# Kernel optimization log

Measured on AMD Instinct MI355X. Metric: run time of the kernel, lower is better.

## Reference

```python
import jax, jax.numpy as jnp
import numpy as np

DIM, H, KV, HD, WIN = 1024, 16, 4, 64, 512
EPS = 1e-6


def rmsnorm(x, w, eps=EPS):
    # torch.nn.RMSNorm: x * rsqrt(mean(x^2, -1) + eps) * w
    return x * jax.lax.rsqrt(jnp.mean(x * x, axis=-1, keepdims=True) + eps) * w


def setup_inputs() -> dict:
    key = jax.random.key(0)
    ks = jax.random.split(key, 7)
    B, T = 4, 2048
    s = 0.02
    return {
        "x": jax.random.normal(ks[0], (B, T, DIM), dtype=jnp.float32),
        "wq": jax.random.normal(ks[1], (H * HD, DIM), dtype=jnp.float32) * s,
        "wk": jax.random.normal(ks[2], (KV * HD, DIM), dtype=jnp.float32) * s,
        "wv": jax.random.normal(ks[3], (KV * HD, DIM), dtype=jnp.float32) * s,
        "wo": jax.random.normal(ks[4], (DIM, H * HD), dtype=jnp.float32) * s,
        "q_norm_w": jnp.ones((HD,), dtype=jnp.float32),
        "k_norm_w": jnp.ones((HD,), dtype=jnp.float32),
    }


def reference(x, wq, wk, wv, wo, q_norm_w, k_norm_w):
    B, T, D = x.shape
    rep = H // KV
    q = (x @ wq.T).reshape(B, T, H, HD)
    k = (x @ wk.T).reshape(B, T, KV, HD)
    v = (x @ wv.T).reshape(B, T, KV, HD)
    q = rmsnorm(q, q_norm_w)
    k = rmsnorm(k, k_norm_w)
    # GQA repeat: each kv head repeated `rep` times contiguously
    k = jnp.repeat(k, rep, axis=2)  # [B,T,H,HD]
    v = jnp.repeat(v, rep, axis=2)
    # scores [B,H,T,T]
    scores = jnp.einsum('bqhd,bkhd->bhqk', q, k) / jnp.sqrt(jnp.float32(HD))
    i = jnp.arange(T)[:, None]
    j = jnp.arange(T)[None, :]
    mask = (i >= j) & (i - j < WIN)  # causal sliding window band
    scores = jnp.where(mask, scores, -jnp.inf)
    attn = jax.nn.softmax(scores, axis=-1)
    y = jnp.einsum('bhqk,bkhd->bqhd', attn, v).reshape(B, T, H * HD)
    return y @ wo.T
```

## Files before the change

kernel.cpp:

```cpp
#include <hip/hip_runtime.h>
#include <hip/hip_bf16.h>

#define DIMD 1024
#define NH   16
#define NKV  4
#define HDIM 64
#define WINSZ 512
#define BB   4
#define TT   2048
#define MROWS (BB*TT)
#define NQKV 1536

typedef __attribute__((ext_vector_type(8))) short short8;
typedef __attribute__((ext_vector_type(4))) float f32x4;

static __device__ __forceinline__ short f2bf(float f) {
  __hip_bfloat16 h = __float2bfloat16(f);
  return __builtin_bit_cast(short, h);
}
static __device__ __forceinline__ float bf2f(short s) {
  return __bfloat162float(__builtin_bit_cast(__hip_bfloat16, s));
}
static __device__ __forceinline__ unsigned pk2(float a, float b) {
  unsigned lo = (unsigned short)f2bf(a);
  unsigned hi = (unsigned short)f2bf(b);
  return lo | (hi << 16);
}

static __device__ __forceinline__ void gld_lds16(const void* g, void* l) {
  __builtin_amdgcn_global_load_lds(
      (const __attribute__((address_space(1))) unsigned int*)g,
      (__attribute__((address_space(3))) unsigned int*)l, 16, 0, 0);
}

template<int N>
static __device__ __forceinline__ float dpp_ror(float x) {
  return __builtin_bit_cast(float, __builtin_amdgcn_update_dpp(
      0, __builtin_bit_cast(int, x), 0x120 + N, 0xF, 0xF, true));
}

__global__ __launch_bounds__(256) void cvt_all_kernel(
    const float* __restrict__ x, const float* __restrict__ wq,
    const float* __restrict__ wk, const float* __restrict__ wv,
    const float* __restrict__ wo,
    short* __restrict__ xb, short* __restrict__ wqkvb, short* __restrict__ wob) {
  size_t u = (size_t)blockIdx.x * 256 + threadIdx.x;
  const float* src; short* dst;
  if (u < 2097152)                   { src = x;  dst = xb; }
  else if ((u -= 2097152) < 262144)  { src = wq; dst = wqkvb; }
  else if ((u -= 262144) < 65536)    { src = wk; dst = wqkvb + 1024*1024; }
  else if ((u -= 65536) < 65536)     { src = wv; dst = wqkvb + 1280*1024; }
  else { u -= 65536;                   src = wo; dst = wob; }
  float4 v = ((const float4*)src)[u];
  short4 o;
  o.x = f2bf(v.x); o.y = f2bf(v.y); o.z = f2bf(v.z); o.w = f2bf(v.w);
  ((short4*)dst)[u] = o;
}

#define BMT 128
#define BNT 128
#define BKT 64

template<bool OUT_BF16>
__global__ __launch_bounds__(256) void gemm_bt(
    const short* __restrict__ A, const short* __restrict__ Bw,
    void* __restrict__ Cout, int M, int N, int K) {
  __shared__ __align__(16) short As[BMT*BKT];
  __shared__ __align__(16) short Bs[BNT*BKT];

  int nwg  = gridDim.x;
  int orig = blockIdx.x;
  int wg   = (orig & 7) * (nwg >> 3) + (orig >> 3);
  int tiles_n = N / BNT;
  int m0 = (wg / tiles_n) * BMT;
  int n0 = (wg % tiles_n) * BNT;

  int tid = threadIdx.x;
  int lane = tid & 63, wv = tid >> 6;
  int l15 = lane & 15, lg = lane >> 4;
  int wr = wv >> 1, wc = wv & 1;

  f32x4 acc[4][4] = {};

  for (int k0 = 0; k0 < K; k0 += BKT) {
    __syncthreads();
    const char* Abase = (const char*)(A + (size_t)m0 * K + k0);
    const char* Bbase = (const char*)(Bw + (size_t)n0 * K + k0);
#pragma unroll
    for (int i = 0; i < 4; ++i) {
      int idx = i * 256 + tid;
      int row = idx >> 3;
      int cb  = (idx & 7) << 4;
      int scb = cb ^ ((row & 7) << 4);
      gld_lds16(Abase + (size_t)row * (K * 2) + scb,
                (char*)As + ((i * 256 + wv * 64) << 4));
      gld_lds16(Bbase + (size_t)row * (K * 2) + scb,
                (char*)Bs + ((i * 256 + wv * 64) << 4));
    }
    __syncthreads();

#pragma unroll
    for (int kk = 0; kk < 2; ++kk) {
      short8 af[4], bfr[4];
      int kb = (kk * 32 + lg * 8) * 2;
#pragma unroll
      for (int mi = 0; mi < 4; ++mi) {
        int row = wr * 64 + mi * 16 + l15;
        af[mi] = *(const short8*)((const char*)As + row * 128 + (kb ^ ((row & 7) << 4)));
      }
#pragma unroll
      for (int ni = 0; ni < 4; ++ni) {
        int row = wc * 64 + ni * 16 + l15;
        bfr[ni] = *(const short8*)((const char*)Bs + row * 128 + (kb ^ ((row & 7) << 4)));
      }
#pragma unroll
      for (int mi = 0; mi < 4; ++mi)
#pragma unroll
        for (int ni = 0; ni < 4; ++ni)
          acc[mi][ni] = __builtin_amdgcn_mfma_f32_16x16x32_bf16(af[mi], bfr[ni], acc[mi][ni], 0, 0, 0);
    }
  }

  int crow0 = m0 + wr * 64, ccol0 = n0 + wc * 64;
#pragma unroll
  for (int mi = 0; mi < 4; ++mi)
#pragma unroll
    for (int ni = 0; ni < 4; ++ni)
#pragma unroll
      for (int r = 0; r < 4; ++r) {
        int row = crow0 + mi * 16 + lg * 4 + r;
        int col = ccol0 + ni * 16 + l15;
        float v = acc[mi][ni][r];
        if (OUT_BF16) ((short*)Cout)[(size_t)row * N + col] = f2bf(v);
        else          ((float*)Cout)[(size_t)row * N + col] = v;
      }
}

__global__ __launch_bounds__(256) void qk_norm_kernel(
    const short* __restrict__ qkv, const float* __restrict__ qw,
    const float* __restrict__ kw, short* __restrict__ Qh, short* __restrict__ Kh) {
  unsigned gid = blockIdx.x * 16u + (threadIdx.x >> 4);
  int l = threadIdx.x & 15;
  unsigned row = gid / 20u;
  int s = (int)(gid - row * 20u);
  int b = row >> 11, t = row & 2047;
  bool isq = s < 16;
  int col = isq ? s * 64 : 1024 + (s - 16) * 64;
  const short* rp = qkv + (size_t)row * NQKV + col + l * 4;
  short4 v4 = *(const short4*)rp;
  float f0 = bf2f(v4.x), f1 = bf2f(v4.y), f2 = bf2f(v4.z), f3 = bf2f(v4.w);
  float ss = f0 * f0 + f1 * f1 + f2 * f2 + f3 * f3;
  ss += dpp_ror<1>(ss); ss += dpp_ror<2>(ss);
  ss += dpp_ror<4>(ss); ss += dpp_ror<8>(ss);
  float r = rsqrtf(ss * (1.0f / 64.0f) + 1e-6f);
  float4 w4 = *(const float4*)((isq ? qw : kw) + l * 4);
  short4 o;
  o.x = f2bf(f0 * r * w4.x); o.y = f2bf(f1 * r * w4.y);
  o.z = f2bf(f2 * r * w4.z); o.w = f2bf(f3 * r * w4.w);
  if (isq) *(short4*)(Qh + (((size_t)b * NH + s) * TT + t) * HDIM + l * 4) = o;
  else     *(short4*)(Kh + (((size_t)b * NKV + (s - 16)) * TT + t) * HDIM + l * 4) = o;
}

__global__ __launch_bounds__(256) void vtrans_kernel(
    const short* __restrict__ qkv, short* __restrict__ Vt) {
  int tb = blockIdx.x, kv = blockIdx.y, b = blockIdx.z;
  __shared__ short tile[64][72];
  int tid = threadIdx.x;
#pragma unroll
  for (int i = 0; i < 2; ++i) {
    int idx = i * 256 + tid;
    int tr = idx >> 3;
    int c8 = (idx & 7) * 8;
    int t = tb * 64 + tr;
    const short* src = qkv + (size_t)(b * TT + t) * NQKV + 1280 + kv * 64 + c8;
    short8 v = *(const short8*)src;
#pragma unroll
    for (int j = 0; j < 8; ++j) tile[tr][c8 + j] = v[j];
  }
  __syncthreads();
#pragma unroll
  for (int i = 0; i < 2; ++i) {
    int idx = i * 256 + tid;
    int d = idx >> 3;
    int t8 = (idx & 7) * 8;
    short8 o;
#pragma unroll
    for (int j = 0; j < 8; ++j) o[j] = tile[t8 + j][d];
    short* dst = Vt + (((size_t)(b * NKV + kv) * HDIM) + d) * TT + tb * 64 + t8;
    *(short8*)dst = o;
  }
}

#define C1A 0.180336880f
#define C2A 11.5415603f

__global__ __launch_bounds__(256) void attn_kernel(
    const short* __restrict__ Qh, const short* __restrict__ Kh,
    const short* __restrict__ Vt, short* __restrict__ Y) {
  int wgid = blockIdx.x;
  int qh = wgid >> 4;
  int kvh = (wgid >> 2) & 3;
  int b = wgid & 3;
  int tid = threadIdx.x, lane = tid & 63, wv = tid >> 6;
  int l15 = lane & 15, lg = lane >> 4;
  int h = kvh * 4 + wv;
  int q0 = qh * 32;
  const short* Qp = Qh + (((size_t)b * NH + h) * TT + q0) * HDIM;
  const char*  Kp = (const char*)(Kh + ((size_t)b * NKV + kvh) * TT * HDIM);
  const char*  Vp = (const char*)(Vt + ((size_t)b * NKV + kvh) * HDIM * TT);

  short8 aqA0 = *(const short8*)(Qp + l15 * HDIM + lg * 8);
  short8 aqA1 = *(const short8*)(Qp + l15 * HDIM + 32 + lg * 8);
  short8 aqB0 = *(const short8*)(Qp + (16 + l15) * HDIM + lg * 8);
  short8 aqB1 = *(const short8*)(Qp + (16 + l15) * HDIM + 32 + lg * 8);

  float lpA = 0.f, lpB = 0.f;
  f32x4 yA[4] = {}, yB[4] = {};

  __shared__ __align__(16) char smem[34816];
  char* Kbuf = smem;
  char* Vbuf = smem + 8192;
  short* PA = (short*)(smem + 16384 + wv * 4608);
  short* PB = PA + 1152;

  int lo = q0 - (WINSZ - 1); if (lo < 0) lo = 0;
  int klo = lo & ~63;
  int nt = (q0 + 32 - klo + 63) >> 6;

  int qiA = q0 + l15, qiB = qiA + 16;

  for (int t = 0; t < nt; ++t) {
    int kc = klo + t * 64;
    __syncthreads();
#pragma unroll
    for (int r = 0; r < 2; ++r) {
      int rr = wv * 16 + r * 8 + (lane >> 3);
      int cb = (lane & 7) * 16;
      int scb = cb ^ ((rr & 7) << 4);
      gld_lds16(Kp + (size_t)(kc + rr) * 128 + scb,
                Kbuf + wv * 2048 + r * 1024);
      gld_lds16(Vp + (size_t)rr * (TT * 2) + kc * 2 + scb,
                Vbuf + wv * 2048 + r * 1024);
    }
    __syncthreads();

    int sw = (l15 & 7) << 4;
    short8 bk0[4], bk1[4];
#pragma unroll
    for (int nc = 0; nc < 4; ++nc) {
      int rb = (nc * 16 + l15) * 128;
      bk0[nc] = *(const short8*)(Kbuf + rb + ((lg * 16) ^ sw));
      bk1[nc] = *(const short8*)(Kbuf + rb + ((lg * 16 + 64) ^ sw));
    }
    short8 bv0[4], bv1[4];
#pragma unroll
    for (int dt = 0; dt < 4; ++dt) {
      int rb = (dt * 16 + l15) * 128;
      bv0[dt] = *(const short8*)(Vbuf + rb + ((lg * 16) ^ sw));
      bv1[dt] = *(const short8*)(Vbuf + rb + ((lg * 16 + 64) ^ sw));
    }
    f32x4 sA[4], sB[4];
    __builtin_amdgcn_s_setprio(1);
#pragma unroll
    for (int nc = 0; nc < 4; ++nc) {
      f32x4 zA = {}, zB = {};
      zA = __builtin_amdgcn_mfma_f32_16x16x32_bf16(bk0[nc], aqA0, zA, 0, 0, 0);
      zB = __builtin_amdgcn_mfma_f32_16x16x32_bf16(bk0[nc], aqB0, zB, 0, 0, 0);
      zA = __builtin_amdgcn_mfma_f32_16x16x32_bf16(bk1[nc], aqA1, zA, 0, 0, 0);
      zB = __builtin_amdgcn_mfma_f32_16x16x32_bf16(bk1[nc], aqB1, zB, 0, 0, 0);
      sA[nc] = zA; sB[nc] = zB;
    }
    __builtin_amdgcn_s_setprio(0);
    bool intA = (kc >= q0 - 496) && (kc + 63 <= q0);
    bool intB = (kc >= q0 - 480) && (kc + 63 <= q0 + 16);
    if (intA && intB) {
#pragma unroll
      for (int nc = 0; nc < 4; ++nc) {
        float pa0 = __builtin_amdgcn_exp2f(fmaf(sA[nc][0], C1A, -C2A));
        float pa1 = __builtin_amdgcn_exp2f(fmaf(sA[nc][1], C1A, -C2A));
        float pa2 = __builtin_amdgcn_exp2f(fmaf(sA[nc][2], C1A, -C2A));
        float pa3 = __builtin_amdgcn_exp2f(fmaf(sA[nc][3], C1A, -C2A));
        float pb0 = __builtin_amdgcn_exp2f(fmaf(sB[nc][0], C1A, -C2A));
        float pb1 = __builtin_amdgcn_exp2f(fmaf(sB[nc][1], C1A, -C2A));
        float pb2 = __builtin_amdgcn_exp2f(fmaf(sB[nc][2], C1A, -C2A));
        float pb3 = __builtin_amdgcn_exp2f(fmaf(sB[nc][3], C1A, -C2A));
        lpA += (pa0 + pa1) + (pa2 + pa3);
        lpB += (pb0 + pb1) + (pb2 + pb3);
        *(uint2*)(PA + l15 * 72 + nc * 16 + lg * 4) = uint2{pk2(pa0, pa1), pk2(pa2, pa3)};
        *(uint2*)(PB + l15 * 72 + nc * 16 + lg * 4) = uint2{pk2(pb0, pb1), pk2(pb2, pb3)};
      }
    } else {
      int kjb = kc + lg * 4;
#pragma unroll
      for (int nc = 0; nc < 4; ++nc) {
        float pa[4], pb[4];
#pragma unroll
        for (int r = 0; r < 4; ++r) {
          int kj = kjb + nc * 16 + r;
          bool okA = (kj <= qiA) && (qiA - kj < WINSZ);
          bool okB = (kj <= qiB) && (qiB - kj < WINSZ);
          pa[r] = okA ? __builtin_amdgcn_exp2f(fmaf(sA[nc][r], C1A, -C2A)) : 0.f;
          pb[r] = okB ? __builtin_amdgcn_exp2f(fmaf(sB[nc][r], C1A, -C2A)) : 0.f;
        }
        lpA += (pa[0] + pa[1]) + (pa[2] + pa[3]);
        lpB += (pb[0] + pb[1]) + (pb[2] + pb[3]);
        *(uint2*)(PA + l15 * 72 + nc * 16 + lg * 4) = uint2{pk2(pa[0], pa[1]), pk2(pa[2], pa[3])};
        *(uint2*)(PB + l15 * 72 + nc * 16 + lg * 4) = uint2{pk2(pb[0], pb[1]), pk2(pb[2], pb[3])};
      }
    }
    short8 apA0 = *(const short8*)(PA + l15 * 72 + lg * 8);
    short8 apA1 = *(const short8*)(PA + l15 * 72 + 32 + lg * 8);
    short8 apB0 = *(const short8*)(PB + l15 * 72 + lg * 8);
    short8 apB1 = *(const short8*)(PB + l15 * 72 + 32 + lg * 8);
    __builtin_amdgcn_s_setprio(1);
#pragma unroll
    for (int dt = 0; dt < 4; ++dt) {
      yA[dt] = __builtin_amdgcn_mfma_f32_16x16x32_bf16(apA0, bv0[dt], yA[dt], 0, 0, 0);
      yB[dt] = __builtin_amdgcn_mfma_f32_16x16x32_bf16(apB0, bv0[dt], yB[dt], 0, 0, 0);
      yA[dt] = __builtin_amdgcn_mfma_f32_16x16x32_bf16(apA1, bv1[dt], yA[dt], 0, 0, 0);
      yB[dt] = __builtin_amdgcn_mfma_f32_16x16x32_bf16(apB1, bv1[dt], yB[dt], 0, 0, 0);
    }
    __builtin_amdgcn_s_setprio(0);
  }

  lpA += __shfl_xor(lpA, 16); lpA += __shfl_xor(lpA, 32);
  lpB += __shfl_xor(lpB, 16); lpB += __shfl_xor(lpB, 32);
  float invqA = 1.0f / lpA;
  float invqB = 1.0f / lpB;
#pragma unroll
  for (int r = 0; r < 4; ++r) {
    float invA = __builtin_bit_cast(float, __builtin_amdgcn_ds_bpermute(
        (lg * 4 + r) << 2, __builtin_bit_cast(int, invqA)));
    float invB = __builtin_bit_cast(float, __builtin_amdgcn_ds_bpermute(
        (lg * 4 + r) << 2, __builtin_bit_cast(int, invqB)));
    int qiAo = q0 + lg * 4 + r, qiBo = qiAo + 16;
#pragma unroll
    for (int dt = 0; dt < 4; ++dt) {
      Y[((size_t)(b * TT + qiAo)) * DIMD + h * HDIM + dt * 16 + l15] = f2bf(yA[dt][r] * invA);
      Y[((size_t)(b * TT + qiBo)) * DIMD + h * HDIM + dt * 16 + l15] = f2bf(yB[dt][r] * invB);
    }
  }
}

extern "C" void kernel_launch(void* const* d_in, const int* in_sizes, int n_in,
                              void* d_out, int out_size, void* d_ws, size_t ws_size,
                              hipStream_t stream) {
  const float* x  = (const float*)d_in[0];
  const float* wq = (const float*)d_in[1];
  const float* wk = (const float*)d_in[2];
  const float* wv = (const float*)d_in[3];
  const float* wo = (const float*)d_in[4];
  const float* qw = (const float*)d_in[5];
  const float* kw = (const float*)d_in[6];

  char* ws = (char*)d_ws;
  short* xb    = (short*)(ws + 0);
  short* wqkvb = (short*)(ws + 16777216);
  short* wob   = (short*)(ws + 19922944);
  short* qkv   = (short*)(ws + 22020096);
  short* Qh    = (short*)(ws + 47185920);
  short* Kh    = (short*)(ws + 63963136);
  short* Vt    = (short*)(ws + 68157440);
  short* Y     = xb;
  float* outp  = (float*)d_out;

  cvt_all_kernel<<<10752, 256, 0, stream>>>(x, wq, wk, wv, wo, xb, wqkvb, wob);
  gemm_bt<true><<<dim3(64 * 12), 256, 0, stream>>>(xb, wqkvb, (void*)qkv, MROWS, NQKV, DIMD);
  qk_norm_kernel<<<10240, 256, 0, stream>>>(qkv, qw, kw, Qh, Kh);
  vtrans_kernel<<<dim3(32, 4, 4), 256, 0, stream>>>(qkv, Vt);
  attn_kernel<<<1024, 256, 0, stream>>>(Qh, Kh, Vt, Y);
  gemm_bt<false><<<dim3(64 * 8), 256, 0, stream>>>(Y, wob, (void*)outp, MROWS, DIMD, DIMD);
}
```

Measured before the change: 120.0 us.

## Merge qk-norm and V-transpose launches; load 128-key tiles per barrier in attention

Combines the QK RMSNorm kernel and the V transpose kernel into one launch, with block index ranges selecting the role, which removes one kernel launch and its gap. The attention kernel now stages 128 keys of K and V per pair of barriers instead of 64 and processes them as two 64-key sub-steps, halving the number of block-wide syncs and load phases. When the last chunk holds only 64 keys, the extra loads are redirected to duplicate valid rows. Shared memory grows from about 34KB to 50KB, which may reduce how many blocks fit on each CU.

```diff
diff --git a/kernel.cpp b/kernel.cpp
--- a/kernel.cpp
+++ b/kernel.cpp
@@ -136,58 +136,59 @@
       }
 }
 
-__global__ __launch_bounds__(256) void qk_norm_kernel(
+__global__ __launch_bounds__(256) void norm_vtrans_kernel(
     const short* __restrict__ qkv, const float* __restrict__ qw,
-    const float* __restrict__ kw, short* __restrict__ Qh, short* __restrict__ Kh) {
-  unsigned gid = blockIdx.x * 16u + (threadIdx.x >> 4);
-  int l = threadIdx.x & 15;
-  unsigned row = gid / 20u;
-  int s = (int)(gid - row * 20u);
-  int b = row >> 11, t = row & 2047;
-  bool isq = s < 16;
-  int col = isq ? s * 64 : 1024 + (s - 16) * 64;
-  const short* rp = qkv + (size_t)row * NQKV + col + l * 4;
-  short4 v4 = *(const short4*)rp;
-  float f0 = bf2f(v4.x), f1 = bf2f(v4.y), f2 = bf2f(v4.z), f3 = bf2f(v4.w);
-  float ss = f0 * f0 + f1 * f1 + f2 * f2 + f3 * f3;
-  ss += dpp_ror<1>(ss); ss += dpp_ror<2>(ss);
-  ss += dpp_ror<4>(ss); ss += dpp_ror<8>(ss);
-  float r = rsqrtf(ss * (1.0f / 64.0f) + 1e-6f);
-  float4 w4 = *(const float4*)((isq ? qw : kw) + l * 4);
-  short4 o;
-  o.x = f2bf(f0 * r * w4.x); o.y = f2bf(f1 * r * w4.y);
-  o.z = f2bf(f2 * r * w4.z); o.w = f2bf(f3 * r * w4.w);
-  if (isq) *(short4*)(Qh + (((size_t)b * NH + s) * TT + t) * HDIM + l * 4) = o;
-  else     *(short4*)(Kh + (((size_t)b * NKV + (s - 16)) * TT + t) * HDIM + l * 4) = o;
-}
-
-__global__ __launch_bounds__(256) void vtrans_kernel(
-    const short* __restrict__ qkv, short* __restrict__ Vt) {
-  int tb = blockIdx.x, kv = blockIdx.y, b = blockIdx.z;
+    const float* __restrict__ kw, short* __restrict__ Qh,
+    short* __restrict__ Kh, short* __restrict__ Vt) {
   __shared__ short tile[64][72];
-  int tid = threadIdx.x;
-#pragma unroll
-  for (int i = 0; i < 2; ++i) {
-    int idx = i * 256 + tid;
-    int tr = idx >> 3;
-    int c8 = (idx & 7) * 8;
-    int t = tb * 64 + tr;
-    const short* src = qkv + (size_t)(b * TT + t) * NQKV + 1280 + kv * 64 + c8;
-    short8 v = *(const short8*)src;
-#pragma unroll
-    for (int j = 0; j < 8; ++j) tile[tr][c8 + j] = v[j];
-  }
-  __syncthreads();
-#pragma unroll
-  for (int i = 0; i < 2; ++i) {
-    int idx = i * 256 + tid;
-    int d = idx >> 3;
-    int t8 = (idx & 7) * 8;
-    short8 o;
-#pragma unroll
-    for (int j = 0; j < 8; ++j) o[j] = tile[t8 + j][d];
-    short* dst = Vt + (((size_t)(b * NKV + kv) * HDIM) + d) * TT + tb * 64 + t8;
-    *(short8*)dst = o;
+  if (blockIdx.x < 10240) {
+    unsigned gid = blockIdx.x * 16u + (threadIdx.x >> 4);
+    int l = threadIdx.x & 15;
+    unsigned row = gid / 20u;
+    int s = (int)(gid - row * 20u);
+    int b = row >> 11, t = row & 2047;
+    bool isq = s < 16;
+    int col = isq ? s * 64 : 1024 + (s - 16) * 64;
+    const short* rp = qkv + (size_t)row * NQKV + col + l * 4;
+    short4 v4 = *(const short4*)rp;
+    float f0 = bf2f(v4.x), f1 = bf2f(v4.y), f2 = bf2f(v4.z), f3 = bf2f(v4.w);
+    float ss = f0 * f0 + f1 * f1 + f2 * f2 + f3 * f3;
+    ss += dpp_ror<1>(ss); ss += dpp_ror<2>(ss);
+    ss += dpp_ror<4>(ss); ss += dpp_ror<8>(ss);
+    float r = rsqrtf(ss * (1.0f / 64.0f) + 1e-6f);
+    float4 w4 = *(const float4*)((isq ? qw : kw) + l * 4);
+    short4 o;
+    o.x = f2bf(f0 * r * w4.x); o.y = f2bf(f1 * r * w4.y);
+    o.z = f2bf(f2 * r * w4.z); o.w = f2bf(f3 * r * w4.w);
+    if (isq) *(short4*)(Qh + (((size_t)b * NH + s) * TT + t) * HDIM + l * 4) = o;
+    else     *(short4*)(Kh + (((size_t)b * NKV + (s - 16)) * TT + t) * HDIM + l * 4) = o;
+  } else {
+    int vi = blockIdx.x - 10240;
+    int tb = vi & 31, kv = (vi >> 5) & 3, b = vi >> 7;
+    int tid = threadIdx.x;
+#pragma unroll
+    for (int i = 0; i < 2; ++i) {
+      int idx = i * 256 + tid;
+      int tr = idx >> 3;
+      int c8 = (idx & 7) * 8;
+      int t = tb * 64 + tr;
+      const short* src = qkv + (size_t)(b * TT + t) * NQKV + 1280 + kv * 64 + c8;
+      short8 v = *(const short8*)src;
+#pragma unroll
+      for (int j = 0; j < 8; ++j) tile[tr][c8 + j] = v[j];
+    }
+    __syncthreads();
+#pragma unroll
+    for (int i = 0; i < 2; ++i) {
+      int idx = i * 256 + tid;
+      int d = idx >> 3;
+      int t8 = (idx & 7) * 8;
+      short8 o;
+#pragma unroll
+      for (int j = 0; j < 8; ++j) o[j] = tile[t8 + j][d];
+      short* dst = Vt + (((size_t)(b * NKV + kv) * HDIM) + d) * TT + tb * 64 + t8;
+      *(short8*)dst = o;
+    }
   }
 }
 
@@ -217,110 +218,119 @@
   float lpA = 0.f, lpB = 0.f;
   f32x4 yA[4] = {}, yB[4] = {};
 
-  __shared__ __align__(16) char smem[34816];
+  __shared__ __align__(16) char smem[51200];
   char* Kbuf = smem;
-  char* Vbuf = smem + 8192;
-  short* PA = (short*)(smem + 16384 + wv * 4608);
+  char* Vbuf = smem + 16384;
+  short* PA = (short*)(smem + 32768 + wv * 4608);
   short* PB = PA + 1152;
 
   int lo = q0 - (WINSZ - 1); if (lo < 0) lo = 0;
   int klo = lo & ~63;
-  int nt = (q0 + 32 - klo + 63) >> 6;
+  int khi = q0 + 32;
 
   int qiA = q0 + l15, qiB = qiA + 16;
 
-  for (int t = 0; t < nt; ++t) {
-    int kc = klo + t * 64;
-    __syncthreads();
-#pragma unroll
-    for (int r = 0; r < 2; ++r) {
-      int rr = wv * 16 + r * 8 + (lane >> 3);
-      int cb = (lane & 7) * 16;
-      int scb = cb ^ ((rr & 7) << 4);
-      gld_lds16(Kp + (size_t)(kc + rr) * 128 + scb,
-                Kbuf + wv * 2048 + r * 1024);
-      gld_lds16(Vp + (size_t)rr * (TT * 2) + kc * 2 + scb,
-                Vbuf + wv * 2048 + r * 1024);
+  for (int kc0 = klo; kc0 < khi; kc0 += 128) {
+    bool two = (kc0 + 64 < khi);
+    __syncthreads();
+#pragma unroll
+    for (int r = 0; r < 4; ++r) {
+      int rrk = wv * 32 + r * 8 + (lane >> 3);
+      int cbk = (lane & 7) * 16;
+      int rowk = (!two && rrk >= 64) ? (rrk - 64) : rrk;
+      gld_lds16(Kp + (size_t)(kc0 + rowk) * 128 + (cbk ^ ((rowk & 7) << 4)),
+                Kbuf + wv * 4096 + r * 1024);
+      int rrv = wv * 16 + r * 4 + (lane >> 4);
+      int cbv = (lane & 15) * 16;
+      int scbv = cbv ^ ((rrv & 7) << 4);
+      int adj = (!two && (cbv & 128)) ? 128 : 0;
+      gld_lds16(Vp + (size_t)rrv * (TT * 2) + kc0 * 2 + scbv - adj,
+                Vbuf + wv * 4096 + r * 1024);
     }
     __syncthreads();
 
     int sw = (l15 & 7) << 4;
-    short8 bk0[4], bk1[4];
-#pragma unroll
-    for (int nc = 0; nc < 4; ++nc) {
-      int rb = (nc * 16 + l15) * 128;
-      bk0[nc] = *(const short8*)(Kbuf + rb + ((lg * 16) ^ sw));
-      bk1[nc] = *(const short8*)(Kbuf + rb + ((lg * 16 + 64) ^ sw));
-    }
-    short8 bv0[4], bv1[4];
-#pragma unroll
-    for (int dt = 0; dt < 4; ++dt) {
-      int rb = (dt * 16 + l15) * 128;
-      bv0[dt] = *(const short8*)(Vbuf + rb + ((lg * 16) ^ sw));
-      bv1[dt] = *(const short8*)(Vbuf + rb + ((lg * 16 + 64) ^ sw));
-    }
-    f32x4 sA[4], sB[4];
-    __builtin_amdgcn_s_setprio(1);
-#pragma unroll
-    for (int nc = 0; nc < 4; ++nc) {
-      f32x4 zA = {}, zB = {};
-      zA = __builtin_amdgcn_mfma_f32_16x16x32_bf16(bk0[nc], aqA0, zA, 0, 0, 0);
-      zB = __builtin_amdgcn_mfma_f32_16x16x32_bf16(bk0[nc], aqB0, zB, 0, 0, 0);
-      zA = __builtin_amdgcn_mfma_f32_16x16x32_bf16(bk1[nc], aqA1, zA, 0, 0, 0);
-      zB = __builtin_amdgcn_mfma_f32_16x16x32_bf16(bk1[nc], aqB1, zB, 0, 0, 0);
-      sA[nc] = zA; sB[nc] = zB;
-    }
-    __builtin_amdgcn_s_setprio(0);
-    bool intA = (kc >= q0 - 496) && (kc + 63 <= q0);
-    bool intB = (kc >= q0 - 480) && (kc + 63 <= q0 + 16);
-    if (intA && intB) {
+#pragma unroll
+    for (int ts = 0; ts < 2; ++ts) {
+      if (ts && !two) break;
+      int kc = kc0 + ts * 64;
+      short8 bk0[4], bk1[4];
 #pragma unroll
       for (int nc = 0; nc < 4; ++nc) {
-        float pa0 = __builtin_amdgcn_exp2f(fmaf(sA[nc][0], C1A, -C2A));
-        float pa1 = __builtin_amdgcn_exp2f(fmaf(sA[nc][1], C1A, -C2A));
-        float pa2 = __builtin_amdgcn_exp2f(fmaf(sA[nc][2], C1A, -C2A));
-        float pa3 = __builtin_amdgcn_exp2f(fmaf(sA[nc][3], C1A, -C2A));
-        float pb0 = __builtin_amdgcn_exp2f(fmaf(sB[nc][0], C1A, -C2A));
-        float pb1 = __builtin_amdgcn_exp2f(fmaf(sB[nc][1], C1A, -C2A));
-        float pb2 = __builtin_amdgcn_exp2f(fmaf(sB[nc][2], C1A, -C2A));
-        float pb3 = __builtin_amdgcn_exp2f(fmaf(sB[nc][3], C1A, -C2A));
-        lpA += (pa0 + pa1) + (pa2 + pa3);
-        lpB += (pb0 + pb1) + (pb2 + pb3);
-        *(uint2*)(PA + l15 * 72 + nc * 16 + lg * 4) = uint2{pk2(pa0, pa1), pk2(pa2, pa3)};
-        *(uint2*)(PB + l15 * 72 + nc * 16 + lg * 4) = uint2{pk2(pb0, pb1), pk2(pb2, pb3)};
-      }
-    } else {
-      int kjb = kc + lg * 4;
+        int rb = (ts * 64 + nc * 16 + l15) * 128;
+        bk0[nc] = *(const short8*)(Kbuf + rb + ((lg * 16) ^ sw));
+        bk1[nc] = *(const short8*)(Kbuf + rb + ((lg * 16 + 64) ^ sw));
+      }
+      short8 bv0[4], bv1[4];
+#pragma unroll
+      for (int dt = 0; dt < 4; ++dt) {
+        int rb = (dt * 16 + l15) * 256 + ts * 128;
+        bv0[dt] = *(const short8*)(Vbuf + rb + ((lg * 16) ^ sw));
+        bv1[dt] = *(const short8*)(Vbuf + rb + ((lg * 16 + 64) ^ sw));
+      }
+      f32x4 sA[4], sB[4];
+      __builtin_amdgcn_s_setprio(1);
 #pragma unroll
       for (int nc = 0; nc < 4; ++nc) {
-        float pa[4], pb[4];
-#pragma unroll
-        for (int r = 0; r < 4; ++r) {
-          int kj = kjb + nc * 16 + r;
-          bool okA = (kj <= qiA) && (qiA - kj < WINSZ);
-          bool okB = (kj <= qiB) && (qiB - kj < WINSZ);
-          pa[r] = okA ? __builtin_amdgcn_exp2f(fmaf(sA[nc][r], C1A, -C2A)) : 0.f;
-          pb[r] = okB ? __builtin_amdgcn_exp2f(fmaf(sB[nc][r], C1A, -C2A)) : 0.f;
+        f32x4 zA = {}, zB = {};
+        zA = __builtin_amdgcn_mfma_f32_16x16x32_bf16(bk0[nc], aqA0, zA, 0, 0, 0);
+        zB = __builtin_amdgcn_mfma_f32_16x16x32_bf16(bk0[nc], aqB0, zB, 0, 0, 0);
+        zA = __builtin_amdgcn_mfma_f32_16x16x32_bf16(bk1[nc], aqA1, zA, 0, 0, 0);
+        zB = __builtin_amdgcn_mfma_f32_16x16x32_bf16(bk1[nc], aqB1, zB, 0, 0, 0);
+        sA[nc] = zA; sB[nc] = zB;
+      }
+      __builtin_amdgcn_s_setprio(0);
+      bool intA = (kc >= q0 - 496) && (kc + 63 <= q0);
+      bool intB = (kc >= q0 - 480) && (kc + 63 <= q0 + 16);
+      if (intA && intB) {
+#pragma unroll
+        for (int nc = 0; nc < 4; ++nc) {
+          float pa0 = __builtin_amdgcn_exp2f(fmaf(sA[nc][0], C1A, -C2A));
+          float pa1 = __builtin_amdgcn_exp2f(fmaf(sA[nc][1], C1A, -C2A));
+          float pa2 = __builtin_amdgcn_exp2f(fmaf(sA[nc][2], C1A, -C2A));
+          float pa3 = __builtin_amdgcn_exp2f(fmaf(sA[nc][3], C1A, -C2A));
+          float pb0 = __builtin_amdgcn_exp2f(fmaf(sB[nc][0], C1A, -C2A));
+          float pb1 = __builtin_amdgcn_exp2f(fmaf(sB[nc][1], C1A, -C2A));
+          float pb2 = __builtin_amdgcn_exp2f(fmaf(sB[nc][2], C1A, -C2A));
+          float pb3 = __builtin_amdgcn_exp2f(fmaf(sB[nc][3], C1A, -C2A));
+          lpA += (pa0 + pa1) + (pa2 + pa3);
+          lpB += (pb0 + pb1) + (pb2 + pb3);
+          *(uint2*)(PA + l15 * 72 + nc * 16 + lg * 4) = uint2{pk2(pa0, pa1), pk2(pa2, pa3)};
+          *(uint2*)(PB + l15 * 72 + nc * 16 + lg * 4) = uint2{pk2(pb0, pb1), pk2(pb2, pb3)};
         }
-        lpA += (pa[0] + pa[1]) + (pa[2] + pa[3]);
-        lpB += (pb[0] + pb[1]) + (pb[2] + pb[3]);
-        *(uint2*)(PA + l15 * 72 + nc * 16 + lg * 4) = uint2{pk2(pa[0], pa[1]), pk2(pa[2], pa[3])};
-        *(uint2*)(PB + l15 * 72 + nc * 16 + lg * 4) = uint2{pk2(pb[0], pb[1]), pk2(pb[2], pb[3])};
-      }
-    }
-    short8 apA0 = *(const short8*)(PA + l15 * 72 + lg * 8);
-    short8 apA1 = *(const short8*)(PA + l15 * 72 + 32 + lg * 8);
-    short8 apB0 = *(const short8*)(PB + l15 * 72 + lg * 8);
-    short8 apB1 = *(const short8*)(PB + l15 * 72 + 32 + lg * 8);
-    __builtin_amdgcn_s_setprio(1);
-#pragma unroll
-    for (int dt = 0; dt < 4; ++dt) {
-      yA[dt] = __builtin_amdgcn_mfma_f32_16x16x32_bf16(apA0, bv0[dt], yA[dt], 0, 0, 0);
-      yB[dt] = __builtin_amdgcn_mfma_f32_16x16x32_bf16(apB0, bv0[dt], yB[dt], 0, 0, 0);
-      yA[dt] = __builtin_amdgcn_mfma_f32_16x16x32_bf16(apA1, bv1[dt], yA[dt], 0, 0, 0);
-      yB[dt] = __builtin_amdgcn_mfma_f32_16x16x32_bf16(apB1, bv1[dt], yB[dt], 0, 0, 0);
-    }
-    __builtin_amdgcn_s_setprio(0);
+      } else {
+        int kjb = kc + lg * 4;
+#pragma unroll
+        for (int nc = 0; nc < 4; ++nc) {
+          float pa[4], pb[4];
+#pragma unroll
+          for (int r = 0; r < 4; ++r) {
+            int kj = kjb + nc * 16 + r;
+            bool okA = (kj <= qiA) && (qiA - kj < WINSZ);
+            bool okB = (kj <= qiB) && (qiB - kj < WINSZ);
+            pa[r] = okA ? __builtin_amdgcn_exp2f(fmaf(sA[nc][r], C1A, -C2A)) : 0.f;
+            pb[r] = okB ? __builtin_amdgcn_exp2f(fmaf(sB[nc][r], C1A, -C2A)) : 0.f;
+          }
+          lpA += (pa[0] + pa[1]) + (pa[2] + pa[3]);
+          lpB += (pb[0] + pb[1]) + (pb[2] + pb[3]);
+          *(uint2*)(PA + l15 * 72 + nc * 16 + lg * 4) = uint2{pk2(pa[0], pa[1]), pk2(pa[2], pa[3])};
+          *(uint2*)(PB + l15 * 72 + nc * 16 + lg * 4) = uint2{pk2(pb[0], pb[1]), pk2(pb[2], pb[3])};
+        }
+      }
+      short8 apA0 = *(const short8*)(PA + l15 * 72 + lg * 8);
+      short8 apA1 = *(const short8*)(PA + l15 * 72 + 32 + lg * 8);
+      short8 apB0 = *(const short8*)(PB + l15 * 72 + lg * 8);
+      short8 apB1 = *(const short8*)(PB + l15 * 72 + 32 + lg * 8);
+      __builtin_amdgcn_s_setprio(1);
+#pragma unroll
+      for (int dt = 0; dt < 4; ++dt) {
+        yA[dt] = __builtin_amdgcn_mfma_f32_16x16x32_bf16(apA0, bv0[dt], yA[dt], 0, 0, 0);
+        yB[dt] = __builtin_amdgcn_mfma_f32_16x16x32_bf16(apB0, bv0[dt], yB[dt], 0, 0, 0);
+        yA[dt] = __builtin_amdgcn_mfma_f32_16x16x32_bf16(apA1, bv1[dt], yA[dt], 0, 0, 0);
+        yB[dt] = __builtin_amdgcn_mfma_f32_16x16x32_bf16(apB1, bv1[dt], yB[dt], 0, 0, 0);
+      }
+      __builtin_amdgcn_s_setprio(0);
+    }
   }
 
   lpA += __shfl_xor(lpA, 16); lpA += __shfl_xor(lpA, 32);
@@ -366,8 +376,7 @@
 
   cvt_all_kernel<<<10752, 256, 0, stream>>>(x, wq, wk, wv, wo, xb, wqkvb, wob);
   gemm_bt<true><<<dim3(64 * 12), 256, 0, stream>>>(xb, wqkvb, (void*)qkv, MROWS, NQKV, DIMD);
-  qk_norm_kernel<<<10240, 256, 0, stream>>>(qkv, qw, kw, Qh, Kh);
-  vtrans_kernel<<<dim3(32, 4, 4), 256, 0, stream>>>(qkv, Vt);
+  norm_vtrans_kernel<<<10752, 256, 0, stream>>>(qkv, qw, kw, Qh, Kh, Vt);
   attn_kernel<<<1024, 256, 0, stream>>>(Qh, Kh, Vt, Y);
   gemm_bt<false><<<dim3(64 * 8), 256, 0, stream>>>(Y, wob, (void*)outp, MROWS, DIMD, DIMD);
 }
```

Measured after the change: 119.7 us. No clear change (-0.3%).

## Merge QK-norm and V-transpose kernels; split softmax/PV per query half

Applied to the files above, without the earlier changes.

The separate qk_norm and vtrans launches become one kernel, using block index ranges to pick the role, which removes one launch and its drain gap. In the attention inner loop, the A and B query sub-tiles are now handled one after the other, each with its own interior/boundary check and its own PV MFMA pass. The aim is to take the fast unmasked path more often and to interleave exp work with MFMA issue. The merged kernel reserves LDS for every block, including the norm blocks that never use it, and the extra branching adds some control overhead.

```diff
diff --git a/kernel.cpp b/kernel.cpp
--- a/kernel.cpp
+++ b/kernel.cpp
@@ -136,58 +136,59 @@
       }
 }
 
-__global__ __launch_bounds__(256) void qk_norm_kernel(
+__global__ __launch_bounds__(256) void norm_vtrans_kernel(
     const short* __restrict__ qkv, const float* __restrict__ qw,
-    const float* __restrict__ kw, short* __restrict__ Qh, short* __restrict__ Kh) {
-  unsigned gid = blockIdx.x * 16u + (threadIdx.x >> 4);
-  int l = threadIdx.x & 15;
-  unsigned row = gid / 20u;
-  int s = (int)(gid - row * 20u);
-  int b = row >> 11, t = row & 2047;
-  bool isq = s < 16;
-  int col = isq ? s * 64 : 1024 + (s - 16) * 64;
-  const short* rp = qkv + (size_t)row * NQKV + col + l * 4;
-  short4 v4 = *(const short4*)rp;
-  float f0 = bf2f(v4.x), f1 = bf2f(v4.y), f2 = bf2f(v4.z), f3 = bf2f(v4.w);
-  float ss = f0 * f0 + f1 * f1 + f2 * f2 + f3 * f3;
-  ss += dpp_ror<1>(ss); ss += dpp_ror<2>(ss);
-  ss += dpp_ror<4>(ss); ss += dpp_ror<8>(ss);
-  float r = rsqrtf(ss * (1.0f / 64.0f) + 1e-6f);
-  float4 w4 = *(const float4*)((isq ? qw : kw) + l * 4);
-  short4 o;
-  o.x = f2bf(f0 * r * w4.x); o.y = f2bf(f1 * r * w4.y);
-  o.z = f2bf(f2 * r * w4.z); o.w = f2bf(f3 * r * w4.w);
-  if (isq) *(short4*)(Qh + (((size_t)b * NH + s) * TT + t) * HDIM + l * 4) = o;
-  else     *(short4*)(Kh + (((size_t)b * NKV + (s - 16)) * TT + t) * HDIM + l * 4) = o;
-}
-
-__global__ __launch_bounds__(256) void vtrans_kernel(
-    const short* __restrict__ qkv, short* __restrict__ Vt) {
-  int tb = blockIdx.x, kv = blockIdx.y, b = blockIdx.z;
+    const float* __restrict__ kw, short* __restrict__ Qh,
+    short* __restrict__ Kh, short* __restrict__ Vt) {
   __shared__ short tile[64][72];
-  int tid = threadIdx.x;
-#pragma unroll
-  for (int i = 0; i < 2; ++i) {
-    int idx = i * 256 + tid;
-    int tr = idx >> 3;
-    int c8 = (idx & 7) * 8;
-    int t = tb * 64 + tr;
-    const short* src = qkv + (size_t)(b * TT + t) * NQKV + 1280 + kv * 64 + c8;
-    short8 v = *(const short8*)src;
-#pragma unroll
-    for (int j = 0; j < 8; ++j) tile[tr][c8 + j] = v[j];
-  }
-  __syncthreads();
-#pragma unroll
-  for (int i = 0; i < 2; ++i) {
-    int idx = i * 256 + tid;
-    int d = idx >> 3;
-    int t8 = (idx & 7) * 8;
-    short8 o;
-#pragma unroll
-    for (int j = 0; j < 8; ++j) o[j] = tile[t8 + j][d];
-    short* dst = Vt + (((size_t)(b * NKV + kv) * HDIM) + d) * TT + tb * 64 + t8;
-    *(short8*)dst = o;
+  if (blockIdx.x < 10240) {
+    unsigned gid = blockIdx.x * 16u + (threadIdx.x >> 4);
+    int l = threadIdx.x & 15;
+    unsigned row = gid / 20u;
+    int s = (int)(gid - row * 20u);
+    int b = row >> 11, t = row & 2047;
+    bool isq = s < 16;
+    int col = isq ? s * 64 : 1024 + (s - 16) * 64;
+    const short* rp = qkv + (size_t)row * NQKV + col + l * 4;
+    short4 v4 = *(const short4*)rp;
+    float f0 = bf2f(v4.x), f1 = bf2f(v4.y), f2 = bf2f(v4.z), f3 = bf2f(v4.w);
+    float ss = f0 * f0 + f1 * f1 + f2 * f2 + f3 * f3;
+    ss += dpp_ror<1>(ss); ss += dpp_ror<2>(ss);
+    ss += dpp_ror<4>(ss); ss += dpp_ror<8>(ss);
+    float r = rsqrtf(ss * (1.0f / 64.0f) + 1e-6f);
+    float4 w4 = *(const float4*)((isq ? qw : kw) + l * 4);
+    short4 o;
+    o.x = f2bf(f0 * r * w4.x); o.y = f2bf(f1 * r * w4.y);
+    o.z = f2bf(f2 * r * w4.z); o.w = f2bf(f3 * r * w4.w);
+    if (isq) *(short4*)(Qh + (((size_t)b * NH + s) * TT + t) * HDIM + l * 4) = o;
+    else     *(short4*)(Kh + (((size_t)b * NKV + (s - 16)) * TT + t) * HDIM + l * 4) = o;
+  } else {
+    int vi = blockIdx.x - 10240;
+    int tb = vi & 31, kv = (vi >> 5) & 3, b = vi >> 7;
+    int tid = threadIdx.x;
+#pragma unroll
+    for (int i = 0; i < 2; ++i) {
+      int idx = i * 256 + tid;
+      int tr = idx >> 3;
+      int c8 = (idx & 7) * 8;
+      int t = tb * 64 + tr;
+      const short* src = qkv + (size_t)(b * TT + t) * NQKV + 1280 + kv * 64 + c8;
+      short8 v = *(const short8*)src;
+#pragma unroll
+      for (int j = 0; j < 8; ++j) tile[tr][c8 + j] = v[j];
+    }
+    __syncthreads();
+#pragma unroll
+    for (int i = 0; i < 2; ++i) {
+      int idx = i * 256 + tid;
+      int d = idx >> 3;
+      int t8 = (idx & 7) * 8;
+      short8 o;
+#pragma unroll
+      for (int j = 0; j < 8; ++j) o[j] = tile[t8 + j][d];
+      short* dst = Vt + (((size_t)(b * NKV + kv) * HDIM) + d) * TT + tb * 64 + t8;
+      *(short8*)dst = o;
+    }
   }
 }
 
@@ -271,53 +272,75 @@
       sA[nc] = zA; sB[nc] = zB;
     }
     __builtin_amdgcn_s_setprio(0);
+
     bool intA = (kc >= q0 - 496) && (kc + 63 <= q0);
     bool intB = (kc >= q0 - 480) && (kc + 63 <= q0 + 16);
-    if (intA && intB) {
+
+    if (intA) {
 #pragma unroll
       for (int nc = 0; nc < 4; ++nc) {
         float pa0 = __builtin_amdgcn_exp2f(fmaf(sA[nc][0], C1A, -C2A));
         float pa1 = __builtin_amdgcn_exp2f(fmaf(sA[nc][1], C1A, -C2A));
         float pa2 = __builtin_amdgcn_exp2f(fmaf(sA[nc][2], C1A, -C2A));
         float pa3 = __builtin_amdgcn_exp2f(fmaf(sA[nc][3], C1A, -C2A));
+        lpA += (pa0 + pa1) + (pa2 + pa3);
+        *(uint2*)(PA + l15 * 72 + nc * 16 + lg * 4) = uint2{pk2(pa0, pa1), pk2(pa2, pa3)};
+      }
+    } else {
+      int kjb = kc + lg * 4;
+#pragma unroll
+      for (int nc = 0; nc < 4; ++nc) {
+        float pa[4];
+#pragma unroll
+        for (int r = 0; r < 4; ++r) {
+          int kj = kjb + nc * 16 + r;
+          bool okA = (kj <= qiA) && (qiA - kj < WINSZ);
+          pa[r] = okA ? __builtin_amdgcn_exp2f(fmaf(sA[nc][r], C1A, -C2A)) : 0.f;
+        }
+        lpA += (pa[0] + pa[1]) + (pa[2] + pa[3]);
+        *(uint2*)(PA + l15 * 72 + nc * 16 + lg * 4) = uint2{pk2(pa[0], pa[1]), pk2(pa[2], pa[3])};
+      }
+    }
+    short8 apA0 = *(const short8*)(PA + l15 * 72 + lg * 8);
+    short8 apA1 = *(const short8*)(PA + l15 * 72 + 32 + lg * 8);
+    __builtin_amdgcn_s_setprio(1);
+#pragma unroll
+    for (int dt = 0; dt < 4; ++dt) {
+      yA[dt] = __builtin_amdgcn_mfma_f32_16x16x32_bf16(apA0, bv0[dt], yA[dt], 0, 0, 0);
+      yA[dt] = __builtin_amdgcn_mfma_f32_16x16x32_bf16(apA1, bv1[dt], yA[dt], 0, 0, 0);
+    }
+    __builtin_amdgcn_s_setprio(0);
+    if (intB) {
+#pragma unroll
+      for (int nc = 0; nc < 4; ++nc) {
         float pb0 = __builtin_amdgcn_exp2f(fmaf(sB[nc][0], C1A, -C2A));
         float pb1 = __builtin_amdgcn_exp2f(fmaf(sB[nc][1], C1A, -C2A));
         float pb2 = __builtin_amdgcn_exp2f(fmaf(sB[nc][2], C1A, -C2A));
         float pb3 = __builtin_amdgcn_exp2f(fmaf(sB[nc][3], C1A, -C2A));
-        lpA += (pa0 + pa1) + (pa2 + pa3);
         lpB += (pb0 + pb1) + (pb2 + pb3);
-        *(uint2*)(PA + l15 * 72 + nc * 16 + lg * 4) = uint2{pk2(pa0, pa1), pk2(pa2, pa3)};
         *(uint2*)(PB + l15 * 72 + nc * 16 + lg * 4) = uint2{pk2(pb0, pb1), pk2(pb2, pb3)};
       }
     } else {
       int kjb = kc + lg * 4;
 #pragma unroll
       for (int nc = 0; nc < 4; ++nc) {
-        float pa[4], pb[4];
+        float pb[4];
 #pragma unroll
         for (int r = 0; r < 4; ++r) {
           int kj = kjb + nc * 16 + r;
-          bool okA = (kj <= qiA) && (qiA - kj < WINSZ);
           bool okB = (kj <= qiB) && (qiB - kj < WINSZ);
-          pa[r] = okA ? __builtin_amdgcn_exp2f(fmaf(sA[nc][r], C1A, -C2A)) : 0.f;
           pb[r] = okB ? __builtin_amdgcn_exp2f(fmaf(sB[nc][r], C1A, -C2A)) : 0.f;
         }
-        lpA += (pa[0] + pa[1]) + (pa[2] + pa[3]);
         lpB += (pb[0] + pb[1]) + (pb[2] + pb[3]);
-        *(uint2*)(PA + l15 * 72 + nc * 16 + lg * 4) = uint2{pk2(pa[0], pa[1]), pk2(pa[2], pa[3])};
         *(uint2*)(PB + l15 * 72 + nc * 16 + lg * 4) = uint2{pk2(pb[0], pb[1]), pk2(pb[2], pb[3])};
       }
     }
-    short8 apA0 = *(const short8*)(PA + l15 * 72 + lg * 8);
-    short8 apA1 = *(const short8*)(PA + l15 * 72 + 32 + lg * 8);
     short8 apB0 = *(const short8*)(PB + l15 * 72 + lg * 8);
     short8 apB1 = *(const short8*)(PB + l15 * 72 + 32 + lg * 8);
     __builtin_amdgcn_s_setprio(1);
 #pragma unroll
     for (int dt = 0; dt < 4; ++dt) {
-      yA[dt] = __builtin_amdgcn_mfma_f32_16x16x32_bf16(apA0, bv0[dt], yA[dt], 0, 0, 0);
       yB[dt] = __builtin_amdgcn_mfma_f32_16x16x32_bf16(apB0, bv0[dt], yB[dt], 0, 0, 0);
-      yA[dt] = __builtin_amdgcn_mfma_f32_16x16x32_bf16(apA1, bv1[dt], yA[dt], 0, 0, 0);
       yB[dt] = __builtin_amdgcn_mfma_f32_16x16x32_bf16(apB1, bv1[dt], yB[dt], 0, 0, 0);
     }
     __builtin_amdgcn_s_setprio(0);
@@ -366,8 +389,7 @@
 
   cvt_all_kernel<<<10752, 256, 0, stream>>>(x, wq, wk, wv, wo, xb, wqkvb, wob);
   gemm_bt<true><<<dim3(64 * 12), 256, 0, stream>>>(xb, wqkvb, (void*)qkv, MROWS, NQKV, DIMD);
-  qk_norm_kernel<<<10240, 256, 0, stream>>>(qkv, qw, kw, Qh, Kh);
-  vtrans_kernel<<<dim3(32, 4, 4), 256, 0, stream>>>(qkv, Vt);
+  norm_vtrans_kernel<<<10752, 256, 0, stream>>>(qkv, qw, kw, Qh, Kh, Vt);
   attn_kernel<<<1024, 256, 0, stream>>>(Qh, Kh, Vt, Y);
   gemm_bt<false><<<dim3(64 * 8), 256, 0, stream>>>(Y, wob, (void*)outp, MROWS, DIMD, DIMD);
 }
```

New measurement: 122.9 us. 2.4% more time.
